# Kernel tuning notes

Hardware: AMD Instinct MI355X
Metric: run time of the kernel (lower is better)

The kernel has to match this reference:

```python
import jax, jax.numpy as jnp
import numpy as np

M, K, E, N, TOPK = 4096, 1024, 8, 1024, 2

def setup_inputs() -> dict:
    key = jax.random.key(0)
    k1, k2, k3, k4, k5 = jax.random.split(key, 5)
    hidden_states = jax.random.normal(k1, (M, K), dtype=jnp.float32)
    w1 = jax.random.normal(k2, (E, K, 2 * N), dtype=jnp.float32) * 0.02
    w2 = jax.random.normal(k3, (E, N, K), dtype=jnp.float32) * 0.02
    topk_weights = jax.random.uniform(k4, (M, TOPK), dtype=jnp.float32)
    topk_ids = jax.random.randint(k5, (M, TOPK), 0, E, dtype=jnp.int64)
    return {"hidden_states": hidden_states, "w1": w1, "w2": w2,
            "topk_weights": topk_weights, "topk_ids": topk_ids}

def reference(hidden_states, w1, w2, topk_weights, topk_ids):
    # Fused MoE: per expert e, y_e = silu_and_mul(x @ w1[e]) @ w2[e];
    # output[m] = sum_k topk_weights[m,k] * y_{topk_ids[m,k]}[m]
    num_experts = w1.shape[0]
    n = w2.shape[1]

    def expert_step(acc, inputs):
        w1_e, w2_e, e = inputs
        gate_up = hidden_states @ w1_e            # [M, 2N]
        gate, up = gate_up[:, :n], gate_up[:, n:]
        h = jax.nn.silu(gate) * up                 # [M, N]
        y_e = h @ w2_e                             # [M, K]
        # combined routing weight of expert e per token (scatter-free finalize)
        coef = jnp.sum(jnp.where(topk_ids == e, topk_weights, 0.0), axis=1)  # [M]
        return acc + coef[:, None] * y_e, None

    init = jnp.zeros_like(hidden_states)
    out, _ = jax.lax.scan(expert_step, init,
                          (w1, w2, jnp.arange(num_experts, dtype=topk_ids.dtype)))
    return out
```

## Files before the change

kernel.cpp:

```cpp
#include <hip/hip_runtime.h>


#define M_TOK   4096
#define K_DIM   1024
#define N_DIM   1024
#define E_NUM   8
#define NPAIR   8192
#define BM      64
#define ROWS_CAP 8704
#define NROWBLK 136
#define HBLK    32

typedef unsigned short u16;
typedef unsigned int   u32;
typedef __attribute__((ext_vector_type(8))) short bf16x8;
typedef __attribute__((ext_vector_type(4))) float f32x4;

#define GPTR(p) ((const __attribute__((address_space(1))) u32*)(const void*)(p))
#define LPTR(p) ((__attribute__((address_space(3))) u32*)(void*)(p))

__device__ __forceinline__ u16 f2bf(float f) {
  union { float f; u32 u; } v; v.f = f;
  u32 r = v.u + 0x7FFFu + ((v.u >> 16) & 1u);
  return (u16)(r >> 16);
}
__device__ __forceinline__ float bf2f(u16 u) {
  union { u32 u; float f; } v; v.u = ((u32)u) << 16;
  return v.f;
}

__global__ __launch_bounds__(256) void hist_kernel(
    const int* __restrict__ topk_ids, int* __restrict__ blockhist) {
  __shared__ int wcnt[4][E_NUM];
  const int t = threadIdx.x, wave = t >> 6, lane = t & 63;
  int e = topk_ids[blockIdx.x * 256 + t] & 7;
#pragma unroll
  for (int ee = 0; ee < E_NUM; ++ee) {
    unsigned long long m = __ballot(e == ee);
    if (lane == ee) wcnt[wave][ee] = (int)__popcll(m);
  }
  __syncthreads();
  if (t < E_NUM) {
    int s = wcnt[0][t] + wcnt[1][t] + wcnt[2][t] + wcnt[3][t];
    blockhist[blockIdx.x * E_NUM + t] = s;
  }
}

__global__ __launch_bounds__(256) void scan_kernel(
    const int* __restrict__ blockhist, int* __restrict__ baseoff,
    int* __restrict__ pair_token, int* __restrict__ block_expert) {
  __shared__ int cnt[E_NUM], off[E_NUM], pad[E_NUM];
  const int t = threadIdx.x;
  if (t < E_NUM) {
    int run = 0;
    for (int b = 0; b < HBLK; ++b) {
      baseoff[b * E_NUM + t] = run;
      run += blockhist[b * E_NUM + t];
    }
    cnt[t] = run;
  }
  __syncthreads();
  if (t == 0) {
    int run = 0, blk = 0;
    for (int e = 0; e < E_NUM; ++e) {
      off[e] = run;
      int padded = ((cnt[e] + BM - 1) / BM) * BM;
      pad[e] = padded;
      for (int b = 0; b < padded / BM; ++b) block_expert[blk++] = e;
      run += padded;
    }
    for (; blk < NROWBLK; ++blk) block_expert[blk] = -1;
  }
  __syncthreads();
  for (int i = t; i < HBLK * E_NUM; i += 256) baseoff[i] += off[i & 7];
  for (int e = 0; e < E_NUM; ++e) {
    int s = off[e] + cnt[e], epos = off[e] + pad[e];
    for (int r = s + t; r < epos; r += 256) pair_token[r] = 0;
  }
}

__global__ __launch_bounds__(256) void assign_kernel(
    const int* __restrict__ topk_ids, const int* __restrict__ baseoff,
    int* __restrict__ pair_token, int* __restrict__ pos_of) {
  __shared__ int wcnt[4][E_NUM], wbase[4][E_NUM];
  const int t = threadIdx.x, wave = t >> 6, lane = t & 63;
  const int p = blockIdx.x * 256 + t;
  const int e = topk_ids[p] & 7;
  int rank = 0;
#pragma unroll
  for (int ee = 0; ee < E_NUM; ++ee) {
    unsigned long long m = __ballot(e == ee);
    if (e == ee) rank = (int)__popcll(m & ((1ull << lane) - 1ull));
    if (lane == ee) wcnt[wave][ee] = (int)__popcll(m);
  }
  __syncthreads();
  if (t < E_NUM) {
    int run = baseoff[blockIdx.x * E_NUM + t];
    for (int w = 0; w < 4; ++w) { wbase[w][t] = run; run += wcnt[w][t]; }
  }
  __syncthreads();
  int pos = wbase[wave][e] + rank;
  pair_token[pos] = p >> 1;
  pos_of[p] = pos;
}

__global__ __launch_bounds__(256) void convert_kernel(
    const float* __restrict__ in, u16* __restrict__ out) {
  int i = blockIdx.x * 256 + threadIdx.x;
  float4 v = ((const float4*)in)[i];
  ushort4 o;
  o.x = f2bf(v.x); o.y = f2bf(v.y); o.z = f2bf(v.z); o.w = f2bf(v.w);
  ((ushort4*)out)[i] = o;
}

__global__ __launch_bounds__(256) void transpose_convert(
    const float* __restrict__ in, u16* __restrict__ out, int R, int Cc) {
  __shared__ float lds[64][65];
  const float* src = in + (size_t)blockIdx.z * R * Cc;
  u16* dst = out + (size_t)blockIdx.z * R * Cc;
  int r0 = blockIdx.x * 64, c0 = blockIdx.y * 64;
  int t = threadIdx.x;
#pragma unroll
  for (int it = 0; it < 16; ++it) {
    int lin = it * 256 + t;
    int rr = lin >> 6, cc = lin & 63;
    lds[cc][rr] = src[(size_t)(r0 + rr) * Cc + c0 + cc];
  }
  __syncthreads();
#pragma unroll
  for (int it = 0; it < 8; ++it) {
    int lin = it * 512 + t * 2;
    int cc = lin >> 6, rr = lin & 63;
    ushort2 o;
    o.x = f2bf(lds[cc][rr]);
    o.y = f2bf(lds[cc][rr + 1]);
    *(ushort2*)&dst[(size_t)(c0 + cc) * R + r0 + rr] = o;
  }
}

template <bool GATHER, int NB>
__global__ __launch_bounds__(256, NB == 2 ? 3 : 4) void gemm64(
    const u16* __restrict__ A, const u16* __restrict__ Bt, u16* __restrict__ Out,
    const int* __restrict__ pair_token, const int* __restrict__ block_expert) {
  const int e = block_expert[blockIdx.x];
  if (e < 0) return;
  __shared__ __align__(16) u16 As[64 * 64];
  __shared__ __align__(16) u16 Bs[NB * 128 * 64];
  const int tid = threadIdx.x;
  const int wave = tid >> 6;
  const int lane = tid & 63;
  const int srow = wave * 8 + (lane >> 3);
  const int kc = ((lane & 7) ^ (srow & 7)) << 3;

  const u16* ap[2];
#pragma unroll
  for (int is = 0; is < 2; ++is) {
    int rt = is * 32 + srow;
    int grow = blockIdx.x * BM + rt;
    int arow = GATHER ? pair_token[grow] : grow;
    ap[is] = A + (size_t)arow * K_DIM + kc;
  }
  const u16* bp[NB][4];
  const u16* base_e = Bt + (size_t)e * (NB * N_DIM) * K_DIM;
#pragma unroll
  for (int nb = 0; nb < NB; ++nb)
#pragma unroll
    for (int is = 0; is < 4; ++is) {
      int rt = is * 32 + srow;
      int n = nb * N_DIM + blockIdx.y * 128 + rt;
      bp[nb][is] = base_e + (size_t)n * K_DIM + kc;
    }
  u16* alds = As + wave * 512;
  u16* blds = Bs + wave * 512;

  f32x4 acc[NB][4][2];
#pragma unroll
  for (int nb = 0; nb < NB; ++nb)
#pragma unroll
    for (int i = 0; i < 4; ++i)
#pragma unroll
      for (int j = 0; j < 2; ++j) acc[nb][i][j] = f32x4{0.f, 0.f, 0.f, 0.f};

  for (int k0 = 0; k0 < K_DIM; k0 += 64) {
#pragma unroll
    for (int is = 0; is < 2; ++is)
      __builtin_amdgcn_global_load_lds(GPTR(ap[is] + k0), LPTR(alds + is * 2048), 16, 0, 0);
#pragma unroll
    for (int nb = 0; nb < NB; ++nb)
#pragma unroll
      for (int is = 0; is < 4; ++is)
        __builtin_amdgcn_global_load_lds(GPTR(bp[nb][is] + k0), LPTR(blds + nb * 8192 + is * 2048), 16, 0, 0);
    __syncthreads();
#pragma unroll
    for (int ks = 0; ks < 2; ++ks) {
      const int cq = ks * 4 + (lane >> 4);
      bf16x8 af[4], bfr[NB][2];
#pragma unroll
      for (int i = 0; i < 4; ++i) {
        int row = i * 16 + (lane & 15);
        af[i] = *(const bf16x8*)&As[row * 64 + ((cq ^ (row & 7)) << 3)];
      }
#pragma unroll
      for (int nb = 0; nb < NB; ++nb)
#pragma unroll
        for (int j = 0; j < 2; ++j) {
          int n = wave * 32 + j * 16 + (lane & 15);
          bfr[nb][j] = *(const bf16x8*)&Bs[nb * 8192 + n * 64 + ((cq ^ (n & 7)) << 3)];
        }
#pragma unroll
      for (int nb = 0; nb < NB; ++nb)
#pragma unroll
        for (int i = 0; i < 4; ++i)
#pragma unroll
          for (int j = 0; j < 2; ++j)
            acc[nb][i][j] = __builtin_amdgcn_mfma_f32_16x16x32_bf16(af[i], bfr[nb][j], acc[nb][i][j], 0, 0, 0);
    }
    __syncthreads();
  }

  const size_t rbase = (size_t)blockIdx.x * BM + ((lane >> 4) * 4);
  const int cbase = blockIdx.y * 128 + wave * 32 + (lane & 15);
#pragma unroll
  for (int i = 0; i < 4; ++i)
#pragma unroll
    for (int j = 0; j < 2; ++j)
#pragma unroll
      for (int r = 0; r < 4; ++r) {
        float v;
        if (NB == 2) {
          float g = acc[0][i][j][r], u = acc[1][i][j][r];
          v = g * u / (1.f + __expf(-g));
        } else {
          v = acc[0][i][j][r];
        }
        Out[(rbase + i * 16 + r) * N_DIM + cbase + j * 16] = f2bf(v);
      }
}

__global__ __launch_bounds__(256) void gather_kernel(
    const u16* __restrict__ y, const float* __restrict__ tw,
    const int* __restrict__ pos_of, float* __restrict__ out) {
  int m = blockIdx.x;
  int k = threadIdx.x * 4;
  int p0 = pos_of[m * 2 + 0], p1 = pos_of[m * 2 + 1];
  float w0 = tw[m * 2 + 0], w1 = tw[m * 2 + 1];
  ushort4 y0 = *(const ushort4*)&y[(size_t)p0 * 1024 + k];
  ushort4 y1 = *(const ushort4*)&y[(size_t)p1 * 1024 + k];
  float4 o;
  o.x = w0 * bf2f(y0.x) + w1 * bf2f(y1.x);
  o.y = w0 * bf2f(y0.y) + w1 * bf2f(y1.y);
  o.z = w0 * bf2f(y0.z) + w1 * bf2f(y1.z);
  o.w = w0 * bf2f(y0.w) + w1 * bf2f(y1.w);
  *(float4*)&out[(size_t)m * 1024 + k] = o;
}

extern "C" void kernel_launch(void* const* d_in, const int* in_sizes, int n_in,
                              void* d_out, int out_size, void* d_ws, size_t ws_size,
                              hipStream_t stream) {
  const float* hs = (const float*)d_in[0];
  const float* w1 = (const float*)d_in[1];
  const float* w2 = (const float*)d_in[2];
  const float* tw = (const float*)d_in[3];
  const int* tids = (const int*)d_in[4];
  float* out = (float*)d_out;

  char* ws = (char*)d_ws;
  u16* hsb = (u16*)(ws);
  u16* w1t = (u16*)(ws + (size_t)(8u << 20));
  u16* w2t = (u16*)(ws + (size_t)(40u << 20));
  u16* h   = (u16*)(ws + (size_t)(56u << 20));
  u16* y   = (u16*)(ws + (size_t)(76u << 20));
  int* pair_token   = (int*)(ws + (size_t)(96u << 20));
  int* pos_of       = (int*)(ws + (size_t)(96u << 20) + 64 * 1024);
  int* block_expert = (int*)(ws + (size_t)(96u << 20) + 128 * 1024);
  int* blockhist    = (int*)(ws + (size_t)(96u << 20) + 192 * 1024);
  int* baseoff      = (int*)(ws + (size_t)(96u << 20) + 256 * 1024);

  hist_kernel<<<HBLK, 256, 0, stream>>>(tids, blockhist);
  scan_kernel<<<1, 256, 0, stream>>>(blockhist, baseoff, pair_token, block_expert);
  assign_kernel<<<HBLK, 256, 0, stream>>>(tids, baseoff, pair_token, pos_of);
  convert_kernel<<<4096, 256, 0, stream>>>(hs, hsb);
  transpose_convert<<<dim3(16, 32, E_NUM), 256, 0, stream>>>(w1, w1t, 1024, 2048);
  transpose_convert<<<dim3(16, 16, E_NUM), 256, 0, stream>>>(w2, w2t, 1024, 1024);
  gemm64<true, 2><<<dim3(NROWBLK, 8), 256, 0, stream>>>(hsb, w1t, h, pair_token, block_expert);
  gemm64<false, 1><<<dim3(NROWBLK, 8), 256, 0, stream>>>(h, w2t, y, pair_token, block_expert);
  gather_kernel<<<4096, 256, 0, stream>>>(y, tw, pos_of, out);
}
```

Before: 265.4 us.

## Double-buffer LDS tiles in MoE GEMM and remap row-block order

Adds a second LDS buffer so the async global-to-LDS loads for the next K tile are issued before computing on the current one, overlapping memory with MFMA work. It also permutes the row-block index so consecutive workgroups are spread across the row-block range, and lowers the launch-bounds occupancy hints to fit the doubled shared memory. Doubling LDS reduces how many blocks fit per CU. The loop keeps only one barrier per iteration, so it relies on the async load completing before that barrier, which may be a correctness risk.

```diff
diff --git a/kernel.cpp b/kernel.cpp
--- a/kernel.cpp
+++ b/kernel.cpp
@@ -139,13 +139,14 @@
 }
 
 template <bool GATHER, int NB>
-__global__ __launch_bounds__(256, NB == 2 ? 3 : 4) void gemm64(
+__global__ __launch_bounds__(256, NB == 2 ? 2 : 3) void gemm64(
     const u16* __restrict__ A, const u16* __restrict__ Bt, u16* __restrict__ Out,
     const int* __restrict__ pair_token, const int* __restrict__ block_expert) {
-  const int e = block_expert[blockIdx.x];
+  const int bx = ((int)blockIdx.x & 7) * (NROWBLK / 8) + ((int)blockIdx.x >> 3);
+  const int e = block_expert[bx];
   if (e < 0) return;
-  __shared__ __align__(16) u16 As[64 * 64];
-  __shared__ __align__(16) u16 Bs[NB * 128 * 64];
+  __shared__ __align__(16) u16 As[2][64 * 64];
+  __shared__ __align__(16) u16 Bs[2][NB * 128 * 64];
   const int tid = threadIdx.x;
   const int wave = tid >> 6;
   const int lane = tid & 63;
@@ -156,7 +157,7 @@
 #pragma unroll
   for (int is = 0; is < 2; ++is) {
     int rt = is * 32 + srow;
-    int grow = blockIdx.x * BM + rt;
+    int grow = bx * BM + rt;
     int arow = GATHER ? pair_token[grow] : grow;
     ap[is] = A + (size_t)arow * K_DIM + kc;
   }
@@ -170,8 +171,6 @@
       int n = nb * N_DIM + blockIdx.y * 128 + rt;
       bp[nb][is] = base_e + (size_t)n * K_DIM + kc;
     }
-  u16* alds = As + wave * 512;
-  u16* blds = Bs + wave * 512;
 
   f32x4 acc[NB][4][2];
 #pragma unroll
@@ -181,16 +180,26 @@
 #pragma unroll
       for (int j = 0; j < 2; ++j) acc[nb][i][j] = f32x4{0.f, 0.f, 0.f, 0.f};
 
+  auto stage = [&](int buf, int k0) {
+#pragma unroll
+    for (int is = 0; is < 2; ++is)
+      __builtin_amdgcn_global_load_lds(GPTR(ap[is] + k0),
+          LPTR(&As[buf][wave * 512 + is * 2048]), 16, 0, 0);
+#pragma unroll
+    for (int nb = 0; nb < NB; ++nb)
+#pragma unroll
+      for (int is = 0; is < 4; ++is)
+        __builtin_amdgcn_global_load_lds(GPTR(bp[nb][is] + k0),
+            LPTR(&Bs[buf][wave * 512 + nb * 8192 + is * 2048]), 16, 0, 0);
+  };
+
+  stage(0, 0);
+  __syncthreads();
+  int cur = 0;
   for (int k0 = 0; k0 < K_DIM; k0 += 64) {
-#pragma unroll
-    for (int is = 0; is < 2; ++is)
-      __builtin_amdgcn_global_load_lds(GPTR(ap[is] + k0), LPTR(alds + is * 2048), 16, 0, 0);
-#pragma unroll
-    for (int nb = 0; nb < NB; ++nb)
-#pragma unroll
-      for (int is = 0; is < 4; ++is)
-        __builtin_amdgcn_global_load_lds(GPTR(bp[nb][is] + k0), LPTR(blds + nb * 8192 + is * 2048), 16, 0, 0);
-    __syncthreads();
+    if (k0 + 64 < K_DIM) stage(cur ^ 1, k0 + 64);
+    const u16* as = &As[cur][0];
+    const u16* bs = &Bs[cur][0];
 #pragma unroll
     for (int ks = 0; ks < 2; ++ks) {
       const int cq = ks * 4 + (lane >> 4);
@@ -198,14 +207,14 @@
 #pragma unroll
       for (int i = 0; i < 4; ++i) {
         int row = i * 16 + (lane & 15);
-        af[i] = *(const bf16x8*)&As[row * 64 + ((cq ^ (row & 7)) << 3)];
+        af[i] = *(const bf16x8*)&as[row * 64 + ((cq ^ (row & 7)) << 3)];
       }
 #pragma unroll
       for (int nb = 0; nb < NB; ++nb)
 #pragma unroll
         for (int j = 0; j < 2; ++j) {
           int n = wave * 32 + j * 16 + (lane & 15);
-          bfr[nb][j] = *(const bf16x8*)&Bs[nb * 8192 + n * 64 + ((cq ^ (n & 7)) << 3)];
+          bfr[nb][j] = *(const bf16x8*)&bs[nb * 8192 + n * 64 + ((cq ^ (n & 7)) << 3)];
         }
 #pragma unroll
       for (int nb = 0; nb < NB; ++nb)
@@ -216,9 +225,10 @@
             acc[nb][i][j] = __builtin_amdgcn_mfma_f32_16x16x32_bf16(af[i], bfr[nb][j], acc[nb][i][j], 0, 0, 0);
     }
     __syncthreads();
-  }
-
-  const size_t rbase = (size_t)blockIdx.x * BM + ((lane >> 4) * 4);
+    cur ^= 1;
+  }
+
+  const size_t rbase = (size_t)bx * BM + ((lane >> 4) * 4);
   const int cbase = blockIdx.y * 128 + wave * 32 + (lane & 15);
 #pragma unroll
   for (int i = 0; i < 4; ++i)
```

After: 261.6 us. Within noise of the previous version (-1.4%).
